# Optimization experiments

Measured on AMD Instinct MI355X. Metric: run time of the kernel, lower is better.

## Reference

```python
import jax, jax.numpy as jnp
import numpy as np
from jax import lax

D_MODEL = 1024
N_EXPERTS = 8
N_ACTIVE = 2
FFN_HIDDEN = int(D_MODEL * 2.0)


def setup_inputs() -> dict:
    key = jax.random.key(0)
    ks = jax.random.split(key, 7)
    B, T = 2, 2048
    s_in = 1.0 / np.sqrt(D_MODEL)
    s_h = 1.0 / np.sqrt(FFN_HIDDEN)
    return {
        "x": jax.random.normal(ks[0], (B, T, D_MODEL), dtype=jnp.float32),
        # router: torch Linear(d_model, n_experts, bias=False) weight [E, D]
        "router_w": jax.random.uniform(ks[1], (N_EXPERTS, D_MODEL), jnp.float32, -s_in, s_in),
        # stacked expert FFN params: w1 [E, H, D], b1 [E, H], w2 [E, D, H], b2 [E, D]
        "w1": jax.random.uniform(ks[2], (N_EXPERTS, FFN_HIDDEN, D_MODEL), jnp.float32, -s_in, s_in),
        "b1": jax.random.uniform(ks[3], (N_EXPERTS, FFN_HIDDEN), jnp.float32, -s_in, s_in),
        "w2": jax.random.uniform(ks[4], (N_EXPERTS, D_MODEL, FFN_HIDDEN), jnp.float32, -s_h, s_h),
        "b2": jax.random.uniform(ks[5], (N_EXPERTS, D_MODEL), jnp.float32, -s_h, s_h),
    }


def reference(x, router_w, w1, b1, w2, b2):
    B, T, D = x.shape
    N = B * T
    xf = x.reshape(N, D)

    logits = xf @ router_w.T                      # [N, E]
    probs = jax.nn.softmax(logits, axis=-1)       # [N, E]

    # --- aux load-balancing loss (f_i is non-differentiable, from indices) ---
    _, disp_idx = lax.top_k(logits, N_ACTIVE)     # [N, K]
    disp_mask = jax.nn.one_hot(disp_idx, N_EXPERTS, dtype=logits.dtype).sum(axis=1)  # [N, E]
    f_i = disp_mask.sum(axis=0) / (N * N_ACTIVE)  # [E]
    P_i = probs.mean(axis=0)                      # [E]
    aux_loss = N_EXPERTS * jnp.sum(f_i * P_i)

    # --- top-k combine weights, renormalized ---
    topk_w, topk_idx = lax.top_k(probs, N_ACTIVE)                 # [N, K]
    topk_w = topk_w / topk_w.sum(axis=-1, keepdims=True)
    # scatter top-k weights into dense [N, E] combine matrix (zeros elsewhere)
    combine_w = (jax.nn.one_hot(topk_idx, N_EXPERTS, dtype=xf.dtype) * topk_w[..., None]).sum(axis=1)

    # --- expert FFNs, weighted combine (loop over small fixed expert set) ---
    out = jnp.zeros_like(xf)
    for e in range(N_EXPERTS):
        h = jax.nn.silu(xf @ w1[e].T + b1[e])     # [N, H]
        y = h @ w2[e].T + b2[e]                   # [N, D]
        out = out + combine_w[:, e:e + 1] * y

    return out.reshape(B, T, D), aux_loss
```

## Files before the change

kernel.cpp:

```cpp
#include <hip/hip_runtime.h>
#include <cstdint>
#include <cstddef>

#define D_MODEL 1024
#define N_EXPERTS 8
#define FFN_H 2048
#define N_TOK 4096
#define CAP 2048

typedef float f32x4 __attribute__((ext_vector_type(4)));
typedef __bf16 bf16x8 __attribute__((ext_vector_type(8)));

static constexpr size_t XB_OFF   = 0;
static constexpr size_t W1B_OFF  = XB_OFF  + (size_t)N_TOK * D_MODEL * 2;
static constexpr size_t W2B_OFF  = W1B_OFF + (size_t)N_EXPERTS * FFN_H * D_MODEL * 2;
static constexpr size_t HBUF_OFF = W2B_OFF + (size_t)N_EXPERTS * D_MODEL * FFN_H * 2;
static constexpr size_t YBUF_OFF = HBUF_OFF + (size_t)N_EXPERTS * CAP * FFN_H * 2;
static constexpr size_t CNT_OFF  = YBUF_OFF + (size_t)N_EXPERTS * CAP * D_MODEL * 2;
static constexpr size_t TOK_OFF  = CNT_OFF + 64;
static constexpr size_t TAE_OFF  = TOK_OFF + (size_t)N_EXPERTS * CAP * 4;
static constexpr size_t TAW_OFF  = TAE_OFF + (size_t)N_TOK * 4;
static constexpr size_t TAP_OFF  = TAW_OFF + (size_t)N_TOK * 8;
static constexpr size_t TIX_OFF  = TAP_OFF + (size_t)N_TOK * 32;
static constexpr size_t TIW_OFF  = TIX_OFF + (size_t)N_TOK * 8;

__device__ __forceinline__ void async_ld16(const void* g, void* l) {
    __builtin_amdgcn_global_load_lds(
        (const __attribute__((address_space(1))) unsigned int*)g,
        (__attribute__((address_space(3))) unsigned int*)l, 16, 0, 0);
}

__global__ __launch_bounds__(256) void cvt_all_kernel(const float* __restrict__ x,
                                                      const float* __restrict__ w1,
                                                      const float* __restrict__ w2,
                                                      __bf16* __restrict__ xb,
                                                      __bf16* __restrict__ w1b,
                                                      __bf16* __restrict__ w2b) {
    int b = blockIdx.x;
    const float* src; __bf16* dst; size_t base;
    if (b < 2048)        { src = x;  dst = xb;  base = (size_t)b * 2048; }
    else if (b < 10240)  { src = w1; dst = w1b; base = (size_t)(b - 2048) * 2048; }
    else                 { src = w2; dst = w2b; base = (size_t)(b - 10240) * 2048; }
    size_t i = base + (size_t)threadIdx.x * 8;
    float4 a = *reinterpret_cast<const float4*>(src + i);
    float4 c = *reinterpret_cast<const float4*>(src + i + 4);
    bf16x8 r;
    r[0] = (__bf16)a.x; r[1] = (__bf16)a.y; r[2] = (__bf16)a.z; r[3] = (__bf16)a.w;
    r[4] = (__bf16)c.x; r[5] = (__bf16)c.y; r[6] = (__bf16)c.z; r[7] = (__bf16)c.w;
    *reinterpret_cast<bf16x8*>(dst + i) = r;
}

__global__ __launch_bounds__(256) void logits_kernel(const float* __restrict__ x,
                                                     const float* __restrict__ rw,
                                                     int* __restrict__ counts,
                                                     int* __restrict__ tA_e,
                                                     float2* __restrict__ tA_w,
                                                     float* __restrict__ tA_p) {
    __shared__ float4 rws4[N_EXPERTS * D_MODEL / 4];
    int tid = threadIdx.x;
    if (blockIdx.x == 0 && tid < 8) counts[tid] = 0;
    for (int i = tid; i < N_EXPERTS * D_MODEL / 4; i += 256)
        rws4[i] = reinterpret_cast<const float4*>(rw)[i];
    __syncthreads();

    int wave = tid >> 6, lane = tid & 63;
    int t = blockIdx.x * 4 + wave;
    const float4* xr = reinterpret_cast<const float4*>(x + (size_t)t * D_MODEL);
    float acc[8] = {};
#pragma unroll
    for (int i = 0; i < 4; ++i) {
        float4 xv = xr[lane + 64 * i];
#pragma unroll
        for (int e = 0; e < 8; ++e) {
            float4 wv = rws4[e * 256 + lane + 64 * i];
            acc[e] += xv.x * wv.x + xv.y * wv.y + xv.z * wv.z + xv.w * wv.w;
        }
    }
#pragma unroll
    for (int e = 0; e < 8; ++e)
        for (int off = 32; off; off >>= 1) acc[e] += __shfl_xor(acc[e], off);

    float mx = acc[0];
#pragma unroll
    for (int e = 1; e < 8; ++e) mx = fmaxf(mx, acc[e]);
    float p[8], s = 0.f;
#pragma unroll
    for (int e = 0; e < 8; ++e) { p[e] = expf(acc[e] - mx); s += p[e]; }
    float inv = 1.f / s;
#pragma unroll
    for (int e = 0; e < 8; ++e) p[e] *= inv;
    int e0 = 0; float p0 = p[0];
#pragma unroll
    for (int e = 1; e < 8; ++e) if (p[e] > p0) { p0 = p[e]; e0 = e; }
    int e1 = -1; float p1 = -1.f;
#pragma unroll
    for (int e = 0; e < 8; ++e) if (e != e0 && p[e] > p1) { p1 = p[e]; e1 = e; }
    float invw = 1.f / (p0 + p1);

    if (lane == 0) {
        tA_e[t] = e0 | (e1 << 16);
        tA_w[t] = make_float2(p0 * invw, p1 * invw);
#pragma unroll
        for (int e = 0; e < 8; ++e) tA_p[t * 8 + e] = p[e];
    }
}

__global__ __launch_bounds__(256) void bucket_kernel(const int* __restrict__ tA_e,
                                                     const float2* __restrict__ tA_w,
                                                     int* __restrict__ counts,
                                                     int* __restrict__ tok_list,
                                                     int2* __restrict__ tinfo_idx,
                                                     float2* __restrict__ tinfo_w) {
    __shared__ int hist[8], base[8];
    int tid = threadIdx.x;
    if (tid < 8) hist[tid] = 0;
    __syncthreads();
    int t = blockIdx.x * 256 + tid;
    int ee = tA_e[t];
    int e0 = ee & 0xffff, e1 = ee >> 16;
    int r0 = atomicAdd(&hist[e0], 1);
    int r1 = atomicAdd(&hist[e1], 1);
    __syncthreads();
    if (tid < 8) base[tid] = atomicAdd(&counts[tid], hist[tid]);
    __syncthreads();
    int q0 = min(base[e0] + r0, CAP - 1);
    int q1 = min(base[e1] + r1, CAP - 1);
    tok_list[e0 * CAP + q0] = t;
    tok_list[e1 * CAP + q1] = t;
    tinfo_idx[t] = make_int2(e0 * CAP + q0, e1 * CAP + q1);
    tinfo_w[t] = tA_w[t];
}

template <int KDIM, bool PASS2>
__global__ __launch_bounds__(256) void ffn_kernel(const __bf16* __restrict__ A_base,
                                                  const __bf16* __restrict__ B_base,
                                                  const float* __restrict__ bias,
                                                  const int* __restrict__ counts,
                                                  const int* __restrict__ tok_list,
                                                  __bf16* __restrict__ Out_base) {
    constexpr int BROWS = PASS2 ? D_MODEL : FFN_H;
    constexpr int NT = BROWS / 128;
    int bid = blockIdx.x;
    int e = bid & 7;
    int r = bid >> 3;
    int n0 = (r % NT) * 128;
    int m0 = (r / NT) * 128;
    int cnt = min(counts[e], CAP);
    if (m0 >= cnt) return;

    __shared__ __bf16 s_a[128 * 32];
    __shared__ __bf16 s_b[128 * 32];
    __shared__ int s_tok[128];

    int tid = threadIdx.x;
    if (!PASS2 && tid < 128) {
        int slot = min(m0 + tid, cnt - 1);
        s_tok[tid] = tok_list[e * CAP + slot];
    }
    __syncthreads();

    int colk = (tid & 3) * 8;
    const __bf16 *a_src0, *a_src1;
    if (PASS2) {
        int s0 = min(m0 + (tid >> 2), cnt - 1);
        int s1 = min(m0 + 64 + (tid >> 2), cnt - 1);
        a_src0 = A_base + ((size_t)e * CAP + s0) * KDIM + colk;
        a_src1 = A_base + ((size_t)e * CAP + s1) * KDIM + colk;
    } else {
        a_src0 = A_base + (size_t)s_tok[tid >> 2] * KDIM + colk;
        a_src1 = A_base + (size_t)s_tok[64 + (tid >> 2)] * KDIM + colk;
    }
    const __bf16* b_src0 = B_base + ((size_t)e * BROWS + n0 + (tid >> 2)) * KDIM + colk;
    const __bf16* b_src1 = b_src0 + (size_t)64 * KDIM;

    char* lds_a = (char*)s_a + (tid >> 6) * 1024;
    char* lds_b = (char*)s_b + (tid >> 6) * 1024;

    int wv = tid >> 6, lane = tid & 63;
    int wm = wv >> 1, wn = wv & 1;
    int lm = lane & 15, q = lane >> 4;
    int a_base = (wm * 64 + lm) * 32 + q * 8;
    int b_base = (wn * 64 + lm) * 32 + q * 8;

    f32x4 acc[4][4] = {};
    for (int k0 = 0; k0 < KDIM; k0 += 32) {
        async_ld16(a_src0 + k0, lds_a);
        async_ld16(a_src1 + k0, lds_a + 4096);
        async_ld16(b_src0 + k0, lds_b);
        async_ld16(b_src1 + k0, lds_b + 4096);
        __syncthreads();
        bf16x8 af[4], bf[4];
#pragma unroll
        for (int f = 0; f < 4; ++f) {
            af[f] = *reinterpret_cast<const bf16x8*>(&s_a[a_base + f * 16 * 32]);
            bf[f] = *reinterpret_cast<const bf16x8*>(&s_b[b_base + f * 16 * 32]);
        }
#pragma unroll
        for (int fm = 0; fm < 4; ++fm)
#pragma unroll
            for (int fn = 0; fn < 4; ++fn)
                acc[fm][fn] = __builtin_amdgcn_mfma_f32_16x16x32_bf16(af[fm], bf[fn], acc[fm][fn], 0, 0, 0);
        __syncthreads();
    }

#pragma unroll
    for (int fn = 0; fn < 4; ++fn) {
        int n = n0 + wn * 64 + fn * 16 + lm;
        float bv = bias[e * BROWS + n];
#pragma unroll
        for (int fm = 0; fm < 4; ++fm) {
            int rbase = wm * 64 + fm * 16 + q * 4;
#pragma unroll
            for (int i = 0; i < 4; ++i) {
                int row = rbase + i;
                int slot = m0 + row;
                if (slot < cnt) {
                    float v = acc[fm][fn][i] + bv;
                    if (!PASS2) {
                        float sv = v / (1.f + __expf(-v));
                        Out_base[((size_t)e * CAP + slot) * FFN_H + n] = (__bf16)sv;
                    } else {
                        Out_base[((size_t)e * CAP + slot) * D_MODEL + n] = (__bf16)v;
                    }
                }
            }
        }
    }
}

__global__ __launch_bounds__(256) void combine_kernel(const __bf16* __restrict__ ybuf,
                                                      const int2* __restrict__ tinfo_idx,
                                                      const float2* __restrict__ tinfo_w,
                                                      const int* __restrict__ counts,
                                                      const float* __restrict__ tA_p,
                                                      float* __restrict__ out) {
    int tid = threadIdx.x;
    if (blockIdx.x == 0) {
        __shared__ float pacc[8];
        if (tid < 8) pacc[tid] = 0.f;
        __syncthreads();
        float a[8] = {};
        for (int t = tid; t < N_TOK; t += 256) {
            const float4* pp = reinterpret_cast<const float4*>(tA_p + (size_t)t * 8);
            float4 u = pp[0], v = pp[1];
            a[0] += u.x; a[1] += u.y; a[2] += u.z; a[3] += u.w;
            a[4] += v.x; a[5] += v.y; a[6] += v.z; a[7] += v.w;
        }
#pragma unroll
        for (int e = 0; e < 8; ++e) atomicAdd(&pacc[e], a[e]);
        __syncthreads();
        if (tid == 0) {
            float s = 0.f;
#pragma unroll
            for (int e = 0; e < 8; ++e)
                s += ((float)counts[e] / (float)(N_TOK * 2)) * (pacc[e] / (float)N_TOK);
            out[(size_t)N_TOK * D_MODEL] = 8.f * s;
        }
    }
    int t = blockIdx.x * 2 + (tid >> 7);
    int d0 = (tid & 127) * 8;
    int2 ix = tinfo_idx[t];
    float2 w = tinfo_w[t];
    bf16x8 ya = *reinterpret_cast<const bf16x8*>(ybuf + (size_t)ix.x * D_MODEL + d0);
    bf16x8 yb = *reinterpret_cast<const bf16x8*>(ybuf + (size_t)ix.y * D_MODEL + d0);
    float4 o0, o1;
    o0.x = w.x * (float)ya[0] + w.y * (float)yb[0];
    o0.y = w.x * (float)ya[1] + w.y * (float)yb[1];
    o0.z = w.x * (float)ya[2] + w.y * (float)yb[2];
    o0.w = w.x * (float)ya[3] + w.y * (float)yb[3];
    o1.x = w.x * (float)ya[4] + w.y * (float)yb[4];
    o1.y = w.x * (float)ya[5] + w.y * (float)yb[5];
    o1.z = w.x * (float)ya[6] + w.y * (float)yb[6];
    o1.w = w.x * (float)ya[7] + w.y * (float)yb[7];
    float* op = out + (size_t)t * D_MODEL + d0;
    *reinterpret_cast<float4*>(op) = o0;
    *reinterpret_cast<float4*>(op + 4) = o1;
}

extern "C" void kernel_launch(void* const* d_in, const int* in_sizes, int n_in,
                              void* d_out, int out_size, void* d_ws, size_t ws_size,
                              hipStream_t stream) {
    const float* x  = (const float*)d_in[0];
    const float* rw = (const float*)d_in[1];
    const float* w1 = (const float*)d_in[2];
    const float* b1 = (const float*)d_in[3];
    const float* w2 = (const float*)d_in[4];
    const float* b2 = (const float*)d_in[5];
    float* out = (float*)d_out;

    char* ws = (char*)d_ws;
    __bf16* xb    = (__bf16*)(ws + XB_OFF);
    __bf16* w1b   = (__bf16*)(ws + W1B_OFF);
    __bf16* w2b   = (__bf16*)(ws + W2B_OFF);
    __bf16* hbuf  = (__bf16*)(ws + HBUF_OFF);
    __bf16* ybuf  = (__bf16*)(ws + YBUF_OFF);
    int*    counts = (int*)(ws + CNT_OFF);
    int*    tok    = (int*)(ws + TOK_OFF);
    int*    tA_e   = (int*)(ws + TAE_OFF);
    float2* tA_w   = (float2*)(ws + TAW_OFF);
    float*  tA_p   = (float*)(ws + TAP_OFF);
    int2*   tix    = (int2*)(ws + TIX_OFF);
    float2* tiw    = (float2*)(ws + TIW_OFF);

    cvt_all_kernel<<<18432, 256, 0, stream>>>(x, w1, w2, xb, w1b, w2b);
    logits_kernel<<<N_TOK / 4, 256, 0, stream>>>(x, rw, counts, tA_e, tA_w, tA_p);
    bucket_kernel<<<N_TOK / 256, 256, 0, stream>>>(tA_e, tA_w, counts, tok, tix, tiw);

    ffn_kernel<D_MODEL, false><<<8 * (FFN_H / 128) * (CAP / 128), 256, 0, stream>>>(
        xb, w1b, b1, counts, tok, hbuf);
    ffn_kernel<FFN_H, true><<<8 * (D_MODEL / 128) * (CAP / 128), 256, 0, stream>>>(
        hbuf, w2b, b2, counts, tok, ybuf);

    combine_kernel<<<N_TOK / 2, 256, 0, stream>>>(ybuf, tix, tiw, counts, tA_p, out);
}
```

Measured before the change: 344.6 us.

## Fuse conversion, routing and bucketing into one prep kernel; deepen FFN K-step

Merges the bf16 conversion, router logits/softmax/top-2 and token bucketing into a single prep kernel, so 64 routing blocks run alongside the conversion blocks. It also accumulates the per-expert probability sums via atomics instead of a serial reduction in the combine kernel. The FFN GEMM now loads 64-wide K chunks per barrier, halving the number of syncs, and adds a 4-blocks-per-SM launch bound. The costs are more LDS per block, a memset launch, and a serial 16-token loop per wave in the routing blocks that could become a tail.

After: 305.5 us. 11.4% less time.

```diff
diff --git a/kernel.cpp b/kernel.cpp
--- a/kernel.cpp
+++ b/kernel.cpp
@@ -17,11 +17,9 @@
 static constexpr size_t HBUF_OFF = W2B_OFF + (size_t)N_EXPERTS * D_MODEL * FFN_H * 2;
 static constexpr size_t YBUF_OFF = HBUF_OFF + (size_t)N_EXPERTS * CAP * FFN_H * 2;
 static constexpr size_t CNT_OFF  = YBUF_OFF + (size_t)N_EXPERTS * CAP * D_MODEL * 2;
-static constexpr size_t TOK_OFF  = CNT_OFF + 64;
-static constexpr size_t TAE_OFF  = TOK_OFF + (size_t)N_EXPERTS * CAP * 4;
-static constexpr size_t TAW_OFF  = TAE_OFF + (size_t)N_TOK * 4;
-static constexpr size_t TAP_OFF  = TAW_OFF + (size_t)N_TOK * 8;
-static constexpr size_t TIX_OFF  = TAP_OFF + (size_t)N_TOK * 32;
+static constexpr size_t PSUM_OFF = CNT_OFF + 32;
+static constexpr size_t TOK_OFF  = PSUM_OFF + 32;
+static constexpr size_t TIX_OFF  = TOK_OFF + (size_t)N_EXPERTS * CAP * 4;
 static constexpr size_t TIW_OFF  = TIX_OFF + (size_t)N_TOK * 8;
 
 __device__ __forceinline__ void async_ld16(const void* g, void* l) {
@@ -30,114 +28,122 @@
         (__attribute__((address_space(3))) unsigned int*)l, 16, 0, 0);
 }
 
-__global__ __launch_bounds__(256) void cvt_all_kernel(const float* __restrict__ x,
-                                                      const float* __restrict__ w1,
-                                                      const float* __restrict__ w2,
-                                                      __bf16* __restrict__ xb,
-                                                      __bf16* __restrict__ w1b,
-                                                      __bf16* __restrict__ w2b) {
+__global__ __launch_bounds__(256) void prep_kernel(const float* __restrict__ x,
+                                                   const float* __restrict__ rw,
+                                                   const float* __restrict__ w1,
+                                                   const float* __restrict__ w2,
+                                                   __bf16* __restrict__ xb,
+                                                   __bf16* __restrict__ w1b,
+                                                   __bf16* __restrict__ w2b,
+                                                   int* __restrict__ counts,
+                                                   float* __restrict__ psum,
+                                                   int* __restrict__ tok_list,
+                                                   int2* __restrict__ tinfo_idx,
+                                                   float2* __restrict__ tinfo_w) {
+    __shared__ float rws[N_EXPERTS * D_MODEL];
+    __shared__ int s_e0[64], s_e1[64], s_r0[64], s_r1[64];
+    __shared__ float s_w0[64], s_w1[64];
+    __shared__ int hist[8], base[8];
+    __shared__ float pacc[8];
+
+    int tid = threadIdx.x;
     int b = blockIdx.x;
-    const float* src; __bf16* dst; size_t base;
-    if (b < 2048)        { src = x;  dst = xb;  base = (size_t)b * 2048; }
-    else if (b < 10240)  { src = w1; dst = w1b; base = (size_t)(b - 2048) * 2048; }
-    else                 { src = w2; dst = w2b; base = (size_t)(b - 10240) * 2048; }
-    size_t i = base + (size_t)threadIdx.x * 8;
-    float4 a = *reinterpret_cast<const float4*>(src + i);
-    float4 c = *reinterpret_cast<const float4*>(src + i + 4);
-    bf16x8 r;
-    r[0] = (__bf16)a.x; r[1] = (__bf16)a.y; r[2] = (__bf16)a.z; r[3] = (__bf16)a.w;
-    r[4] = (__bf16)c.x; r[5] = (__bf16)c.y; r[6] = (__bf16)c.z; r[7] = (__bf16)c.w;
-    *reinterpret_cast<bf16x8*>(dst + i) = r;
-}
-
-__global__ __launch_bounds__(256) void logits_kernel(const float* __restrict__ x,
-                                                     const float* __restrict__ rw,
-                                                     int* __restrict__ counts,
-                                                     int* __restrict__ tA_e,
-                                                     float2* __restrict__ tA_w,
-                                                     float* __restrict__ tA_p) {
-    __shared__ float4 rws4[N_EXPERTS * D_MODEL / 4];
-    int tid = threadIdx.x;
-    if (blockIdx.x == 0 && tid < 8) counts[tid] = 0;
-    for (int i = tid; i < N_EXPERTS * D_MODEL / 4; i += 256)
-        rws4[i] = reinterpret_cast<const float4*>(rw)[i];
+    if (b >= 64) {
+        int c = b - 64;
+        const float* src; __bf16* dst; size_t bb;
+        if (c < 2048)       { src = x;  dst = xb;  bb = (size_t)c * 2048; }
+        else if (c < 10240) { src = w1; dst = w1b; bb = (size_t)(c - 2048) * 2048; }
+        else                { src = w2; dst = w2b; bb = (size_t)(c - 10240) * 2048; }
+        size_t i = bb + (size_t)tid * 8;
+        float4 a = *reinterpret_cast<const float4*>(src + i);
+        float4 d = *reinterpret_cast<const float4*>(src + i + 4);
+        bf16x8 r;
+        r[0] = (__bf16)a.x; r[1] = (__bf16)a.y; r[2] = (__bf16)a.z; r[3] = (__bf16)a.w;
+        r[4] = (__bf16)d.x; r[5] = (__bf16)d.y; r[6] = (__bf16)d.z; r[7] = (__bf16)d.w;
+        *reinterpret_cast<bf16x8*>(dst + i) = r;
+        return;
+    }
+
+    for (int i = tid * 4; i < N_EXPERTS * D_MODEL; i += 256 * 4)
+        *reinterpret_cast<float4*>(&rws[i]) = *reinterpret_cast<const float4*>(&rw[i]);
+    if (tid < 8) { hist[tid] = 0; pacc[tid] = 0.f; }
     __syncthreads();
 
     int wave = tid >> 6, lane = tid & 63;
-    int t = blockIdx.x * 4 + wave;
-    const float4* xr = reinterpret_cast<const float4*>(x + (size_t)t * D_MODEL);
-    float acc[8] = {};
-#pragma unroll
-    for (int i = 0; i < 4; ++i) {
-        float4 xv = xr[lane + 64 * i];
+    float psacc[8] = {};
+    for (int it = 0; it < 16; ++it) {
+        int li = wave * 16 + it;
+        int t = b * 64 + li;
+        const float* xr = x + (size_t)t * D_MODEL;
+        float acc[8] = {};
+#pragma unroll
+        for (int i = 0; i < D_MODEL / 64; ++i) {
+            float xv = xr[lane + 64 * i];
+#pragma unroll
+            for (int e = 0; e < 8; ++e) acc[e] += xv * rws[e * D_MODEL + lane + 64 * i];
+        }
+        float logit[8];
 #pragma unroll
         for (int e = 0; e < 8; ++e) {
-            float4 wv = rws4[e * 256 + lane + 64 * i];
-            acc[e] += xv.x * wv.x + xv.y * wv.y + xv.z * wv.z + xv.w * wv.w;
-        }
-    }
-#pragma unroll
-    for (int e = 0; e < 8; ++e)
-        for (int off = 32; off; off >>= 1) acc[e] += __shfl_xor(acc[e], off);
-
-    float mx = acc[0];
-#pragma unroll
-    for (int e = 1; e < 8; ++e) mx = fmaxf(mx, acc[e]);
-    float p[8], s = 0.f;
-#pragma unroll
-    for (int e = 0; e < 8; ++e) { p[e] = expf(acc[e] - mx); s += p[e]; }
-    float inv = 1.f / s;
-#pragma unroll
-    for (int e = 0; e < 8; ++e) p[e] *= inv;
-    int e0 = 0; float p0 = p[0];
-#pragma unroll
-    for (int e = 1; e < 8; ++e) if (p[e] > p0) { p0 = p[e]; e0 = e; }
-    int e1 = -1; float p1 = -1.f;
-#pragma unroll
-    for (int e = 0; e < 8; ++e) if (e != e0 && p[e] > p1) { p1 = p[e]; e1 = e; }
-    float invw = 1.f / (p0 + p1);
-
-    if (lane == 0) {
-        tA_e[t] = e0 | (e1 << 16);
-        tA_w[t] = make_float2(p0 * invw, p1 * invw);
-#pragma unroll
-        for (int e = 0; e < 8; ++e) tA_p[t * 8 + e] = p[e];
-    }
-}
-
-__global__ __launch_bounds__(256) void bucket_kernel(const int* __restrict__ tA_e,
-                                                     const float2* __restrict__ tA_w,
-                                                     int* __restrict__ counts,
-                                                     int* __restrict__ tok_list,
-                                                     int2* __restrict__ tinfo_idx,
-                                                     float2* __restrict__ tinfo_w) {
-    __shared__ int hist[8], base[8];
-    int tid = threadIdx.x;
-    if (tid < 8) hist[tid] = 0;
-    __syncthreads();
-    int t = blockIdx.x * 256 + tid;
-    int ee = tA_e[t];
-    int e0 = ee & 0xffff, e1 = ee >> 16;
-    int r0 = atomicAdd(&hist[e0], 1);
-    int r1 = atomicAdd(&hist[e1], 1);
-    __syncthreads();
-    if (tid < 8) base[tid] = atomicAdd(&counts[tid], hist[tid]);
-    __syncthreads();
-    int q0 = min(base[e0] + r0, CAP - 1);
-    int q1 = min(base[e1] + r1, CAP - 1);
-    tok_list[e0 * CAP + q0] = t;
-    tok_list[e1 * CAP + q1] = t;
-    tinfo_idx[t] = make_int2(e0 * CAP + q0, e1 * CAP + q1);
-    tinfo_w[t] = tA_w[t];
+            float v = acc[e];
+            for (int off = 32; off; off >>= 1) v += __shfl_xor(v, off);
+            logit[e] = v;
+        }
+        float mx = logit[0];
+#pragma unroll
+        for (int e = 1; e < 8; ++e) mx = fmaxf(mx, logit[e]);
+        float p[8], s = 0.f;
+#pragma unroll
+        for (int e = 0; e < 8; ++e) { p[e] = expf(logit[e] - mx); s += p[e]; }
+        float inv = 1.f / s;
+#pragma unroll
+        for (int e = 0; e < 8; ++e) { p[e] *= inv; psacc[e] += p[e]; }
+        int e0 = 0; float p0 = p[0];
+#pragma unroll
+        for (int e = 1; e < 8; ++e) if (p[e] > p0) { p0 = p[e]; e0 = e; }
+        int e1 = -1; float p1 = -1.f;
+#pragma unroll
+        for (int e = 0; e < 8; ++e) if (e != e0 && p[e] > p1) { p1 = p[e]; e1 = e; }
+        float invw = 1.f / (p0 + p1);
+        if (lane == 0) {
+            s_e0[li] = e0; s_e1[li] = e1;
+            s_w0[li] = p0 * invw; s_w1[li] = p1 * invw;
+        }
+    }
+    if (lane == 0)
+#pragma unroll
+        for (int e = 0; e < 8; ++e) atomicAdd(&pacc[e], psacc[e]);
+    __syncthreads();
+
+    if (tid < 64) {
+        s_r0[tid] = atomicAdd(&hist[s_e0[tid]], 1);
+        s_r1[tid] = atomicAdd(&hist[s_e1[tid]], 1);
+    }
+    __syncthreads();
+    if (tid < 8) {
+        base[tid] = atomicAdd(&counts[tid], hist[tid]);
+        atomicAdd(&psum[tid], pacc[tid]);
+    }
+    __syncthreads();
+    if (tid < 64) {
+        int t = b * 64 + tid;
+        int e0 = s_e0[tid], e1 = s_e1[tid];
+        int q0 = min(base[e0] + s_r0[tid], CAP - 1);
+        int q1 = min(base[e1] + s_r1[tid], CAP - 1);
+        tok_list[e0 * CAP + q0] = t;
+        tok_list[e1 * CAP + q1] = t;
+        tinfo_idx[t] = make_int2(e0 * CAP + q0, e1 * CAP + q1);
+        tinfo_w[t] = make_float2(s_w0[tid], s_w1[tid]);
+    }
 }
 
 template <int KDIM, bool PASS2>
-__global__ __launch_bounds__(256) void ffn_kernel(const __bf16* __restrict__ A_base,
-                                                  const __bf16* __restrict__ B_base,
-                                                  const float* __restrict__ bias,
-                                                  const int* __restrict__ counts,
-                                                  const int* __restrict__ tok_list,
-                                                  __bf16* __restrict__ Out_base) {
+__global__ __launch_bounds__(256, 4) void ffn_kernel(const __bf16* __restrict__ A_base,
+                                                     const __bf16* __restrict__ B_base,
+                                                     const float* __restrict__ bias,
+                                                     const int* __restrict__ counts,
+                                                     const int* __restrict__ tok_list,
+                                                     __bf16* __restrict__ Out_base) {
     constexpr int BROWS = PASS2 ? D_MODEL : FFN_H;
     constexpr int NT = BROWS / 128;
     int bid = blockIdx.x;
@@ -148,8 +154,8 @@
     int cnt = min(counts[e], CAP);
     if (m0 >= cnt) return;
 
-    __shared__ __bf16 s_a[128 * 32];
-    __shared__ __bf16 s_b[128 * 32];
+    __shared__ __bf16 s_a[2][128 * 32];
+    __shared__ __bf16 s_b[2][128 * 32];
     __shared__ int s_tok[128];
 
     int tid = threadIdx.x;
@@ -173,8 +179,8 @@
     const __bf16* b_src0 = B_base + ((size_t)e * BROWS + n0 + (tid >> 2)) * KDIM + colk;
     const __bf16* b_src1 = b_src0 + (size_t)64 * KDIM;
 
-    char* lds_a = (char*)s_a + (tid >> 6) * 1024;
-    char* lds_b = (char*)s_b + (tid >> 6) * 1024;
+    char* lds_a = (char*)&s_a[0][0] + (tid >> 6) * 1024;
+    char* lds_b = (char*)&s_b[0][0] + (tid >> 6) * 1024;
 
     int wv = tid >> 6, lane = tid & 63;
     int wm = wv >> 1, wn = wv & 1;
@@ -183,23 +189,30 @@
     int b_base = (wn * 64 + lm) * 32 + q * 8;
 
     f32x4 acc[4][4] = {};
-    for (int k0 = 0; k0 < KDIM; k0 += 32) {
-        async_ld16(a_src0 + k0, lds_a);
-        async_ld16(a_src1 + k0, lds_a + 4096);
-        async_ld16(b_src0 + k0, lds_b);
-        async_ld16(b_src1 + k0, lds_b + 4096);
+    for (int k0 = 0; k0 < KDIM; k0 += 64) {
+        async_ld16(a_src0 + k0,      lds_a);
+        async_ld16(a_src1 + k0,      lds_a + 4096);
+        async_ld16(a_src0 + k0 + 32, lds_a + 8192);
+        async_ld16(a_src1 + k0 + 32, lds_a + 8192 + 4096);
+        async_ld16(b_src0 + k0,      lds_b);
+        async_ld16(b_src1 + k0,      lds_b + 4096);
+        async_ld16(b_src0 + k0 + 32, lds_b + 8192);
+        async_ld16(b_src1 + k0 + 32, lds_b + 8192 + 4096);
         __syncthreads();
-        bf16x8 af[4], bf[4];
-#pragma unroll
-        for (int f = 0; f < 4; ++f) {
-            af[f] = *reinterpret_cast<const bf16x8*>(&s_a[a_base + f * 16 * 32]);
-            bf[f] = *reinterpret_cast<const bf16x8*>(&s_b[b_base + f * 16 * 32]);
-        }
-#pragma unroll
-        for (int fm = 0; fm < 4; ++fm)
-#pragma unroll
-            for (int fn = 0; fn < 4; ++fn)
-                acc[fm][fn] = __builtin_amdgcn_mfma_f32_16x16x32_bf16(af[fm], bf[fn], acc[fm][fn], 0, 0, 0);
+#pragma unroll
+        for (int kk = 0; kk < 2; ++kk) {
+            bf16x8 af[4], bf[4];
+#pragma unroll
+            for (int f = 0; f < 4; ++f) {
+                af[f] = *reinterpret_cast<const bf16x8*>(&s_a[kk][a_base + f * 16 * 32]);
+                bf[f] = *reinterpret_cast<const bf16x8*>(&s_b[kk][b_base + f * 16 * 32]);
+            }
+#pragma unroll
+            for (int fm = 0; fm < 4; ++fm)
+#pragma unroll
+                for (int fn = 0; fn < 4; ++fn)
+                    acc[fm][fn] = __builtin_amdgcn_mfma_f32_16x16x32_bf16(af[fm], bf[fn], acc[fm][fn], 0, 0, 0);
+        }
         __syncthreads();
     }
 
@@ -232,30 +245,15 @@
                                                       const int2* __restrict__ tinfo_idx,
                                                       const float2* __restrict__ tinfo_w,
                                                       const int* __restrict__ counts,
-                                                      const float* __restrict__ tA_p,
+                                                      const float* __restrict__ psum,
                                                       float* __restrict__ out) {
     int tid = threadIdx.x;
-    if (blockIdx.x == 0) {
-        __shared__ float pacc[8];
-        if (tid < 8) pacc[tid] = 0.f;
-        __syncthreads();
-        float a[8] = {};
-        for (int t = tid; t < N_TOK; t += 256) {
-            const float4* pp = reinterpret_cast<const float4*>(tA_p + (size_t)t * 8);
-            float4 u = pp[0], v = pp[1];
-            a[0] += u.x; a[1] += u.y; a[2] += u.z; a[3] += u.w;
-            a[4] += v.x; a[5] += v.y; a[6] += v.z; a[7] += v.w;
-        }
-#pragma unroll
-        for (int e = 0; e < 8; ++e) atomicAdd(&pacc[e], a[e]);
-        __syncthreads();
-        if (tid == 0) {
-            float s = 0.f;
-#pragma unroll
-            for (int e = 0; e < 8; ++e)
-                s += ((float)counts[e] / (float)(N_TOK * 2)) * (pacc[e] / (float)N_TOK);
-            out[(size_t)N_TOK * D_MODEL] = 8.f * s;
-        }
+    if (blockIdx.x == 0 && tid == 0) {
+        float s = 0.f;
+#pragma unroll
+        for (int e = 0; e < 8; ++e)
+            s += ((float)counts[e] / (float)(N_TOK * 2)) * (psum[e] / (float)N_TOK);
+        out[(size_t)N_TOK * D_MODEL] = 8.f * s;
     }
     int t = blockIdx.x * 2 + (tid >> 7);
     int d0 = (tid & 127) * 8;
@@ -289,27 +287,26 @@
     float* out = (float*)d_out;
 
     char* ws = (char*)d_ws;
-    __bf16* xb    = (__bf16*)(ws + XB_OFF);
-    __bf16* w1b   = (__bf16*)(ws + W1B_OFF);
-    __bf16* w2b   = (__bf16*)(ws + W2B_OFF);
-    __bf16* hbuf  = (__bf16*)(ws + HBUF_OFF);
-    __bf16* ybuf  = (__bf16*)(ws + YBUF_OFF);
+    __bf16* xb     = (__bf16*)(ws + XB_OFF);
+    __bf16* w1b    = (__bf16*)(ws + W1B_OFF);
+    __bf16* w2b    = (__bf16*)(ws + W2B_OFF);
+    __bf16* hbuf   = (__bf16*)(ws + HBUF_OFF);
+    __bf16* ybuf   = (__bf16*)(ws + YBUF_OFF);
     int*    counts = (int*)(ws + CNT_OFF);
+    float*  psum   = (float*)(ws + PSUM_OFF);
     int*    tok    = (int*)(ws + TOK_OFF);
-    int*    tA_e   = (int*)(ws + TAE_OFF);
-    float2* tA_w   = (float2*)(ws + TAW_OFF);
-    float*  tA_p   = (float*)(ws + TAP_OFF);
     int2*   tix    = (int2*)(ws + TIX_OFF);
     float2* tiw    = (float2*)(ws + TIW_OFF);
 
-    cvt_all_kernel<<<18432, 256, 0, stream>>>(x, w1, w2, xb, w1b, w2b);
-    logits_kernel<<<N_TOK / 4, 256, 0, stream>>>(x, rw, counts, tA_e, tA_w, tA_p);
-    bucket_kernel<<<N_TOK / 256, 256, 0, stream>>>(tA_e, tA_w, counts, tok, tix, tiw);
+    hipMemsetAsync(ws + CNT_OFF, 0, 64, stream);
+
+    prep_kernel<<<64 + 18432, 256, 0, stream>>>(x, rw, w1, w2, xb, w1b, w2b,
+                                                counts, psum, tok, tix, tiw);
 
     ffn_kernel<D_MODEL, false><<<8 * (FFN_H / 128) * (CAP / 128), 256, 0, stream>>>(
         xb, w1b, b1, counts, tok, hbuf);
     ffn_kernel<FFN_H, true><<<8 * (D_MODEL / 128) * (CAP / 128), 256, 0, stream>>>(
         hbuf, w2b, b2, counts, tok, ybuf);
 
-    combine_kernel<<<N_TOK / 2, 256, 0, stream>>>(ybuf, tix, tiw, counts, tA_p, out);
-}
+    combine_kernel<<<N_TOK / 2, 256, 0, stream>>>(ybuf, tix, tiw, counts, psum, out);
+}
```
